# Optimization experiments

Hardware: AMD Instinct MI355X
Metric: run time of the kernel (lower is better)

Reference implementation:

```python
import jax, jax.numpy as jnp
import numpy as np

MEM_LEN = 8


def _conv(x, w, b, stride=1):
    y = jax.lax.conv_general_dilated(x, w, (stride, stride), 'VALID',
                                     dimension_numbers=('NCHW', 'OIHW', 'NCHW'))
    return y + b[None, :, None, None]


def _maxpool3s2(x):
    return jax.lax.reduce_window(x, -jnp.inf, jax.lax.max,
                                 (1, 1, 3, 3), (1, 1, 2, 2), 'VALID')


def _relu(x):
    return jax.nn.relu(x)


def setup_inputs() -> dict:
    key = jax.random.key(0)
    ks = jax.random.split(key, 32)

    def w(i, shape):
        fan_in = float(np.prod(shape[1:]))
        return jax.random.normal(ks[i], shape, jnp.float32) * np.float32(1.0 / np.sqrt(fan_in))

    def bias(i, n):
        return jax.random.normal(ks[i], (n,), jnp.float32) * np.float32(0.01)

    return {
        'x': jax.random.normal(ks[0], (1, 287, 287, 3), jnp.float32),
        'z_reg': jax.random.normal(ks[1], (MEM_LEN, 256, 16), jnp.float32) * 0.1,
        'z_cls': jax.random.normal(ks[2], (MEM_LEN, 256, 16), jnp.float32) * 0.1,
        'bb_w1': w(3, (96, 3, 11, 11)),  'bb_b1': bias(4, 96),
        'bb_w2': w(5, (256, 96, 5, 5)),  'bb_b2': bias(6, 256),
        'bb_w3': w(7, (384, 256, 3, 3)), 'bb_b3': bias(8, 384),
        'bb_w4': w(9, (384, 384, 3, 3)), 'bb_b4': bias(10, 384),
        'bb_w5': w(11, (256, 384, 3, 3)), 'bb_b5': bias(12, 256),
        'wr': w(13, (256, 256, 3, 3)), 'br': bias(14, 256),   # conv_reg2 (conv_search of loc)
        'wc': w(15, (256, 256, 3, 3)), 'bc': bias(16, 256),   # conv_cls2 (conv_search of cls)
        'rh_w1': w(17, (256, 256, 1, 1)), 'rh_b1': bias(18, 256),
        'rh_w2': w(19, (20, 256, 1, 1)),  'rh_b2': bias(20, 20),
        'ch_w1': w(21, (256, 256, 1, 1)), 'ch_b1': bias(22, 256),
        'ch_w2': w(23, (10, 256, 1, 1)),  'ch_b2': bias(24, 10),
        'anc0': jax.random.normal(ks[25], (MEM_LEN, 2205), jnp.float32) * 10.0,
        'anc1': jax.random.normal(ks[26], (MEM_LEN, 2205), jnp.float32) * 10.0,
        'anc2': jax.random.uniform(ks[27], (MEM_LEN, 2205), jnp.float32) * 80.0 + 20.0,
        'anc3': jax.random.uniform(ks[28], (MEM_LEN, 2205), jnp.float32) * 80.0 + 20.0,
    }


def reference(x, z_reg, z_cls,
              bb_w1, bb_b1, bb_w2, bb_b2, bb_w3, bb_b3, bb_w4, bb_b4, bb_w5, bb_b5,
              wr, br, wc, bc,
              rh_w1, rh_b1, rh_w2, rh_b2, ch_w1, ch_b1, ch_w2, ch_b2,
              anc0, anc1, anc2, anc3):
    # Backbone (AlexNet features, BN folded into biases)
    xp = jnp.transpose(x, (0, 3, 1, 2))                     # (1,3,287,287)
    h = _relu(_maxpool3s2(_conv(xp, bb_w1, bb_b1, 2)))      # (1,96,69,69)
    h = _relu(_maxpool3s2(_conv(h, bb_w2, bb_b2)))          # (1,256,32,32)
    h = _relu(_conv(h, bb_w3, bb_b3))                       # (1,384,30,30)
    h = _relu(_conv(h, bb_w4, bb_b4))                       # (1,384,28,28)
    xf = _conv(h, bb_w5, bb_b5)                             # (1,256,26,26)

    c_x = _relu(_conv(xf, wr, br))                          # conv_reg2 -> (1,256,24,24)
    r_x = _relu(_conv(xf, wc, bc))                          # conv_cls2 -> (1,256,24,24)

    def unfold44(t):                                        # (1,256,24,24) -> (256,16,441)
        p = jax.lax.conv_general_dilated_patches(
            t.reshape(256, 1, 24, 24), (4, 4), (1, 1), 'VALID',
            dimension_numbers=('NCHW', 'OIHW', 'NCHW'))     # (256,16,21,21)
        return p.reshape(256, 16, 441)

    c_p = unfold44(c_x)
    r_p = unfold44(r_x)

    # Batched cross-correlation over mem_len templates (fuses the original python loop)
    zr = z_reg.reshape(MEM_LEN, 256, 16)
    zc = z_cls.reshape(MEM_LEN, 256, 16)
    reg_corr = jnp.einsum('ckl,mck->mcl', r_p, zr).reshape(MEM_LEN, 256, 21, 21)
    cls_corr = jnp.einsum('ckl,mck->mcl', c_p, zc).reshape(MEM_LEN, 256, 21, 21)

    cls = _conv(_relu(_conv(cls_corr, ch_w1, ch_b1)), ch_w2, ch_b2)   # (M,10,21,21)
    reg = _conv(_relu(_conv(reg_corr, rh_w1, rh_b1)), rh_w2, rh_b2)   # (M,20,21,21)

    score = jax.nn.softmax(cls.reshape(MEM_LEN, 2, -1), axis=1)       # (M,2,2205)
    delta = reg.reshape(MEM_LEN, 4, -1)                               # (M,4,2205)

    d0 = delta[:, 0, :] * anc2 + anc0
    d1 = delta[:, 1, :] * anc3 + anc1
    d2 = jnp.exp(delta[:, 2, :]) * anc2
    d3 = jnp.exp(delta[:, 3, :]) * anc3
    return (d0, d1, d2, d3, score[:, 1, :])
```

## Files before the change

kernel.cpp:

```cpp
#include <hip/hip_runtime.h>
#include <math.h>

#define TPB 256
static inline int cdiv(int a, int b) { return (a + b - 1) / b; }

typedef short bf8 __attribute__((ext_vector_type(8)));
typedef float f4 __attribute__((ext_vector_type(4)));

__device__ inline float b2f(unsigned short u) {
    union { unsigned int i; float f; } v; v.i = ((unsigned int)u) << 16; return v.f;
}
__device__ inline short f2b(float f) {
    union { float f; unsigned int u; } v; v.f = f;
    unsigned int r = v.u + 0x7FFF + ((v.u >> 16) & 1);
    return (short)(r >> 16);
}

#define OW1   0
#define OW2   67584
#define OW3   722944
#define OW4   1607680
#define OW5   2934784
#define OWRC  3819520
#define OWH1  4999168
#define OZT   5130240
#define OWH2  5195776
#define OBIAS 5203456
#define OACT1 5205504
#define OP1   7062368
#define OACTB 7521472
#define OXF   9520064
#define OCRC  9695168

#define ACT2_OFF  0
#define POOL2_OFF 1083648
#define ACT3_OFF  1347840
#define ACT4_OFF  1695488

__global__ __launch_bounds__(256) void wprep_k(
        const float* __restrict__ bb_w1, const float* __restrict__ bb_w2,
        const float* __restrict__ bb_w3, const float* __restrict__ bb_w4,
        const float* __restrict__ bb_w5,
        const float* __restrict__ wr, const float* __restrict__ wc,
        const float* __restrict__ ch_w1, const float* __restrict__ rh_w1,
        const float* __restrict__ ch_w2, const float* __restrict__ rh_w2,
        const float* __restrict__ z_cls, const float* __restrict__ z_reg,
        const float* __restrict__ br, const float* __restrict__ bc,
        const float* __restrict__ chb1, const float* __restrict__ rhb1,
        const float* __restrict__ x,
        short* __restrict__ W, float* __restrict__ biasf,
        short* __restrict__ xb) {
    __shared__ float lds[3465];
    int bid = blockIdx.x;
    int t = threadIdx.x;

    if (bid < 1792) {
        const float* src;
        short* dst;
        int C, K2, Ot, KwC, orow;
        if (bid < 384)       { int o = bid;        C = 256; K2 = 9;  src = bb_w3 + (size_t)o * 2304; dst = W + OW3;  Ot = 384; KwC = 768;  orow = o; }
        else if (bid < 768)  { int o = bid - 384;  C = 384; K2 = 9;  src = bb_w4 + (size_t)o * 3456; dst = W + OW4;  Ot = 384; KwC = 1152; orow = o; }
        else if (bid < 1024) { int o = bid - 768;  C = 384; K2 = 9;  src = bb_w5 + (size_t)o * 3456; dst = W + OW5;  Ot = 256; KwC = 1152; orow = o; }
        else if (bid < 1280) { int o = bid - 1024; C = 256; K2 = 9;  src = wr    + (size_t)o * 2304; dst = W + OWRC; Ot = 512; KwC = 768;  orow = o; }
        else if (bid < 1536) { int o = bid - 1280; C = 256; K2 = 9;  src = wc    + (size_t)o * 2304; dst = W + OWRC; Ot = 512; KwC = 768;  orow = o + 256; }
        else                 { int o = bid - 1536; C = 96;  K2 = 25; src = bb_w2 + (size_t)o * 2400; dst = W + OW2;  Ot = 256; KwC = 512;  orow = o; }

        int n = C * K2;
        int Cp = C + 1;
        if (K2 == 9) {
            for (int i = t; i < n; i += 256) {
                int kk = i % 9, c = i / 9;
                lds[kk * Cp + c] = src[i];
            }
            __syncthreads();
#pragma unroll
            for (int kk = 0; kk < 9; ++kk) {
                int ki = kk / 3, kj = kk % 3;
                short* rowb = dst + ((size_t)ki * Ot + orow) * KwC + kj * C;
                for (int c = t; c < C; c += 256)
                    rowb[c] = f2b(lds[kk * Cp + c]);
            }
        } else {
            for (int i = t; i < n; i += 256) {
                int kk = i % 25, c = i / 25;
                lds[kk * Cp + c] = src[i];
            }
            __syncthreads();
            for (int kk = 0; kk < 25; ++kk) {
                int ki = kk / 5, kj = kk % 5;
                short* rowb = dst + ((size_t)ki * Ot + orow) * KwC + kj * C;
                if (t < C) rowb[t] = f2b(lds[kk * Cp + t]);
            }
            if (t < 160) {
                int ki = t / 32, kp = 480 + (t & 31);
                dst[((size_t)ki * Ot + orow) * KwC + kp] = 0;
            }
        }
        return;
    }

    int fidx = (bid - 1792) * 256 + t;
    if (fidx < 67584) {
        int k = fidx & 63, o = (fidx >> 6) % 96, ki = fidx / (64 * 96);
        float v = 0.f;
        if (k < 33) v = bb_w1[o * 363 + (k % 3) * 121 + ki * 11 + (k / 3)];
        W[fidx] = f2b(v);
    } else if (fidx < 198656) {
        int i = fidx - 67584;
        const float* src = (i < 65536) ? ch_w1 : rh_w1;
        W[OWH1 + i] = f2b(src[i & 65535]);
    } else if (fidx < 206336) {
        int i = fidx - 198656;
        int o = i >> 8, c = i & 255;
        float v = (o < 10) ? ch_w2[o * 256 + c] : rh_w2[(o - 10) * 256 + c];
        W[OWH2 + i] = f2b(v);
    } else if (fidx < 271872) {
        int i = fidx - 206336;
        const float* src = (i < 32768) ? z_cls : z_reg;
        int j = i & 32767;
        int c = j & 255, k = (j >> 8) & 15, m = j >> 12;
        W[OZT + i] = f2b(src[m * 4096 + c * 16 + k]);
    } else if (fidx < 272896) {
        int i = fidx - 271872;
        const float* src = (i < 256) ? br : (i < 512) ? bc : (i < 768) ? chb1 : rhb1;
        biasf[i] = src[i & 255];
    } else {
        int i = fidx - 272896;
        if (i < 247107) xb[i] = f2b(x[i]);
    }
}

template <int BKC>
__global__ __launch_bounds__(256) void gemm_k(
        const short* __restrict__ in, const short* __restrict__ wt,
        const float* __restrict__ bias, short* __restrict__ out,
        int M, int N, int Wo, int CinW, int Cin,
        int S, int SPR, int aWrap, int bWrap, int KwCp,
        int relu, int msplit, int wsec, int bsec, int nt) {
    constexpr int BK = BKC * 32;
    constexpr int LDW = BK + 8;
    constexpr int CPR = BK / 8;
    constexpr int RPR = 256 / CPR;
    __shared__ short sa[2][64 * LDW];
    __shared__ short sb[2][64 * LDW];

    int bid = blockIdx.x;
    int m0 = (bid / nt) * 64, n0 = (bid % nt) * 64;
    int t = threadIdx.x;
    int lane = t & 63;
    int wid = t >> 6, wm = wid >> 1, wn = wid & 1;
    int sec = (m0 >= msplit) ? 1 : 0;
    const short* wts = wt + (size_t)sec * wsec;
    const float* bs = bias + sec * bsec;

    int rql = t / CPR;
    int ch8 = (t % CPR) * 8;

    const short* pA[BKC];
    const short* pB[BKC];
#pragma unroll
    for (int q = 0; q < BKC; ++q) {
        int mr = m0 + q * RPR + rql; if (mr > M - 1) mr = M - 1;
        int oy = mr / Wo, ox = mr - oy * Wo;
        pA[q] = in + (size_t)oy * CinW + (size_t)ox * Cin + ch8;
        int nr = n0 + q * RPR + rql; if (nr > N - 1) nr = N - 1;
        pB[q] = wts + (size_t)nr * KwCp + ch8;
    }
    int swb = rql * LDW + ch8;

    int arow = (wm * 32 + (lane & 15)) * LDW + (lane >> 4) * 8;
    int brow = (wn * 32 + (lane & 15)) * LDW + (lane >> 4) * 8;

    f4 acc[2][2] = {};
    bf8 va0[BKC], vb0[BKC], va1[BKC], vb1[BKC];
    int srow = 0;

#define LOAD_STEP(vaX, vbX)                                                   \
    do {                                                                      \
        _Pragma("unroll")                                                     \
        for (int q = 0; q < BKC; ++q) {                                       \
            vaX[q] = *(const bf8*)pA[q];                                      \
            vbX[q] = *(const bf8*)pB[q];                                      \
        }                                                                     \
        if (++srow == SPR) {                                                  \
            srow = 0;                                                         \
            _Pragma("unroll")                                                 \
            for (int q = 0; q < BKC; ++q) { pA[q] += aWrap; pB[q] += bWrap; } \
        } else {                                                              \
            _Pragma("unroll")                                                 \
            for (int q = 0; q < BKC; ++q) { pA[q] += BK; pB[q] += BK; }       \
        }                                                                     \
    } while (0)

#define WRITE_LDS(buf, vaX, vbX)                                              \
    do {                                                                      \
        _Pragma("unroll")                                                     \
        for (int q = 0; q < BKC; ++q) {                                       \
            *(bf8*)&sa[buf][swb + q * (RPR * LDW)] = vaX[q];                  \
            *(bf8*)&sb[buf][swb + q * (RPR * LDW)] = vbX[q];                  \
        }                                                                     \
    } while (0)

#define MFMA_STEP(buf)                                                        \
    do {                                                                      \
        const short* A = sa[buf];                                             \
        const short* B = sb[buf];                                             \
        _Pragma("unroll")                                                     \
        for (int kc = 0; kc < BKC; ++kc) {                                    \
            bf8 a0 = *(const bf8*)&A[arow + kc * 32];                         \
            bf8 a1 = *(const bf8*)&A[arow + 16 * LDW + kc * 32];              \
            bf8 b0 = *(const bf8*)&B[brow + kc * 32];                         \
            bf8 b1 = *(const bf8*)&B[brow + 16 * LDW + kc * 32];              \
            acc[0][0] = __builtin_amdgcn_mfma_f32_16x16x32_bf16(a0, b0, acc[0][0], 0, 0, 0); \
            acc[0][1] = __builtin_amdgcn_mfma_f32_16x16x32_bf16(a0, b1, acc[0][1], 0, 0, 0); \
            acc[1][0] = __builtin_amdgcn_mfma_f32_16x16x32_bf16(a1, b0, acc[1][0], 0, 0, 0); \
            acc[1][1] = __builtin_amdgcn_mfma_f32_16x16x32_bf16(a1, b1, acc[1][1], 0, 0, 0); \
        }                                                                     \
    } while (0)

    LOAD_STEP(va0, vb0);
    WRITE_LDS(0, va0, vb0);
    if (S > 1) LOAD_STEP(va1, vb1);
    __syncthreads();

    for (int s = 0; s < S; s += 2) {
        if (s + 2 < S) LOAD_STEP(va0, vb0);
        MFMA_STEP(0);
        if (s + 1 < S) WRITE_LDS(1, va1, vb1);
        __syncthreads();
        if (s + 1 >= S) break;
        if (s + 3 < S) LOAD_STEP(va1, vb1);
        MFMA_STEP(1);
        if (s + 2 < S) WRITE_LDS(0, va0, vb0);
        __syncthreads();
    }
#undef LOAD_STEP
#undef WRITE_LDS
#undef MFMA_STEP

#pragma unroll
    for (int i = 0; i < 2; ++i) {
#pragma unroll
        for (int j = 0; j < 2; ++j) {
            int gm_base = m0 + wm * 32 + i * 16 + (lane >> 4) * 4;
            int gn = n0 + wn * 32 + j * 16 + (lane & 15);
            if (gn < N) {
                float bv = bs[gn];
#pragma unroll
                for (int r = 0; r < 4; ++r) {
                    int gm = gm_base + r;
                    if (gm < M) {
                        float v = acc[i][j][r] + bv;
                        if (relu) v = fmaxf(v, 0.f);
                        out[(size_t)gm * N + gn] = f2b(v);
                    }
                }
            }
        }
    }
}

__global__ void pool_k(const short* __restrict__ in, short* __restrict__ out,
                       int C8, int Win, int Ho) {
    int idx = blockIdx.x * blockDim.x + threadIdx.x;
    int total = Ho * Ho * C8;
    if (idx >= total) return;
    int c8 = idx % C8;
    int p = idx / C8;
    int oy = p / Ho, ox = p % Ho;
    int C = C8 * 8;
    float mx[8];
#pragma unroll
    for (int e = 0; e < 8; ++e) mx[e] = -INFINITY;
#pragma unroll
    for (int ki = 0; ki < 3; ++ki)
#pragma unroll
        for (int kj = 0; kj < 3; ++kj) {
            const bf8 v = *(const bf8*)(in + ((size_t)(oy * 2 + ki) * Win + ox * 2 + kj) * C + c8 * 8);
#pragma unroll
            for (int e = 0; e < 8; ++e) mx[e] = fmaxf(mx[e], b2f((unsigned short)v[e]));
        }
    bf8 o;
#pragma unroll
    for (int e = 0; e < 8; ++e) o[e] = f2b(fmaxf(mx[e], 0.f));
    *(bf8*)(out + (size_t)p * C + c8 * 8) = o;
}

__global__ void dwcorr_k(const short* __restrict__ crcb, const short* __restrict__ zt,
                         short* __restrict__ corr) {
    int idx = blockIdx.x * blockDim.x + threadIdx.x;
    if (idx >= 2 * 903168) return;
    int half = idx / 903168;
    int r = idx - half * 903168;
    int c = r & 255;
    int l = (r >> 8) % 441;
    int mb = r / (441 * 256);
    int y = l / 21, xx = l % 21;
    const short* ip = crcb + half * 256 + (size_t)(y * 24 + xx) * 512 + c;
    const short* zp = zt + half * 32768 + mb * 4096 + c;
    float acc = 0.f;
#pragma unroll
    for (int ki = 0; ki < 4; ++ki)
#pragma unroll
        for (int kj = 0; kj < 4; ++kj)
            acc = fmaf(b2f((unsigned short)ip[(ki * 24 + kj) * 512]),
                       b2f((unsigned short)zp[(ki * 4 + kj) * 256]), acc);
    corr[((size_t)(half * 3584 + mb * 441 + l)) * 256 + c] = f2b(acc);
}

__global__ void head2epi_k(const short* __restrict__ hid, const short* __restrict__ wh2,
                           const float* __restrict__ chb2, const float* __restrict__ rhb2,
                           const float* __restrict__ a0, const float* __restrict__ a1,
                           const float* __restrict__ a2, const float* __restrict__ a3,
                           float* __restrict__ out) {
    const int Ntot = 8 * 2205;
    int idx = blockIdx.x * blockDim.x + threadIdx.x;
    if (idx >= 3 * Ntot) return;
    int g = idx / Ntot;
    int r = idx - g * Ntot;
    int m = r / 2205, j = r % 2205;
    int a = j / 441, pos = j % 441;
    int ml = m * 441 + pos;
    const short* h = hid + (size_t)((g == 0) ? ml : 3584 + ml) * 256;
    int row0, row1;
    float acc0, acc1;
    if (g == 0)      { row0 = a;      row1 = 5 + a;  acc0 = chb2[a];      acc1 = chb2[5 + a];  }
    else if (g == 1) { row0 = 10 + a; row1 = 15 + a; acc0 = rhb2[a];      acc1 = rhb2[5 + a];  }
    else             { row0 = 20 + a; row1 = 25 + a; acc0 = rhb2[10 + a]; acc1 = rhb2[15 + a]; }
    const short* w0 = wh2 + row0 * 256;
    const short* w1 = wh2 + row1 * 256;
    for (int c = 0; c < 256; c += 8) {
        bf8 hv = *(const bf8*)(h + c);
        bf8 w0v = *(const bf8*)(w0 + c);
        bf8 w1v = *(const bf8*)(w1 + c);
#pragma unroll
        for (int e = 0; e < 8; ++e) {
            float hf = b2f((unsigned short)hv[e]);
            acc0 = fmaf(hf, b2f((unsigned short)w0v[e]), acc0);
            acc1 = fmaf(hf, b2f((unsigned short)w1v[e]), acc1);
        }
    }
    if (g == 0) {
        out[4 * Ntot + r] = 1.f / (1.f + expf(acc0 - acc1));
    } else if (g == 1) {
        out[0 * Ntot + r] = fmaf(acc0, a2[r], a0[r]);
        out[1 * Ntot + r] = fmaf(acc1, a3[r], a1[r]);
    } else {
        out[2 * Ntot + r] = expf(acc0) * a2[r];
        out[3 * Ntot + r] = expf(acc1) * a3[r];
    }
}

extern "C" void kernel_launch(void* const* d_in, const int* in_sizes, int n_in,
                              void* d_out, int out_size, void* d_ws, size_t ws_size,
                              hipStream_t stream) {
    const float* x     = (const float*)d_in[0];
    const float* z_reg = (const float*)d_in[1];
    const float* z_cls = (const float*)d_in[2];
    const float* bb_w1 = (const float*)d_in[3];
    const float* bb_b1 = (const float*)d_in[4];
    const float* bb_w2 = (const float*)d_in[5];
    const float* bb_b2 = (const float*)d_in[6];
    const float* bb_w3 = (const float*)d_in[7];
    const float* bb_b3 = (const float*)d_in[8];
    const float* bb_w4 = (const float*)d_in[9];
    const float* bb_b4 = (const float*)d_in[10];
    const float* bb_w5 = (const float*)d_in[11];
    const float* bb_b5 = (const float*)d_in[12];
    const float* wr    = (const float*)d_in[13];
    const float* br    = (const float*)d_in[14];
    const float* wc    = (const float*)d_in[15];
    const float* bc    = (const float*)d_in[16];
    const float* rh_w1 = (const float*)d_in[17];
    const float* rh_b1 = (const float*)d_in[18];
    const float* rh_w2 = (const float*)d_in[19];
    const float* rh_b2 = (const float*)d_in[20];
    const float* ch_w1 = (const float*)d_in[21];
    const float* ch_b1 = (const float*)d_in[22];
    const float* ch_w2 = (const float*)d_in[23];
    const float* ch_b2 = (const float*)d_in[24];
    const float* anc0  = (const float*)d_in[25];
    const float* anc1  = (const float*)d_in[26];
    const float* anc2  = (const float*)d_in[27];
    const float* anc3  = (const float*)d_in[28];

    short* sws  = (short*)d_ws;
    short* W    = sws;
    float* biasf = (float*)(sws + OBIAS);
    short* act1 = sws + OACT1;
    short* pool1 = sws + OP1;
    short* actB = sws + OACTB;
    short* xb   = actB;
    short* act2 = actB + ACT2_OFF;
    short* pool2 = actB + POOL2_OFF;
    short* act3 = actB + ACT3_OFF;
    short* act4 = actB + ACT4_OFF;
    short* corr = actB;
    short* xf   = sws + OXF;
    short* crcb = sws + OCRC;
    short* hid  = act1;

    const int BIG = 1 << 30;

    wprep_k<<<1792 + 2032, 256, 0, stream>>>(
        bb_w1, bb_w2, bb_w3, bb_w4, bb_w5, wr, wc, ch_w1, rh_w1, ch_w2, rh_w2,
        z_cls, z_reg, br, bc, ch_b1, rh_b1, x, W, biasf, xb);

    gemm_k<2><<<302 * 2, 256, 0, stream>>>(
        xb, W + OW1, bb_b1, act1,
        19321, 96, 139, 1722, 6,
        11, 1, 861, 6144, 64, 0, BIG, 0, 0, 2);
    pool_k<<<cdiv(69 * 69 * 12, TPB), TPB, 0, stream>>>(act1, pool1, 12, 139, 69);

    gemm_k<4><<<67 * 4, 256, 0, stream>>>(
        pool1, W + OW2, bb_b2, act2,
        4225, 256, 65, 6624, 96,
        20, 4, 6240, 130688, 512, 0, BIG, 0, 0, 4);
    pool_k<<<cdiv(32 * 32 * 32, TPB), TPB, 0, stream>>>(act2, pool2, 32, 65, 32);

    gemm_k<4><<<15 * 6, 256, 0, stream>>>(
        pool2, W + OW3, bb_b3, act3,
        900, 384, 30, 8192, 256,
        18, 6, 7552, 294272, 768, 1, BIG, 0, 0, 6);

    gemm_k<4><<<13 * 6, 256, 0, stream>>>(
        act3, W + OW4, bb_b4, act4,
        784, 384, 28, 11520, 384,
        27, 9, 10496, 441344, 1152, 1, BIG, 0, 0, 6);

    gemm_k<4><<<11 * 4, 256, 0, stream>>>(
        act4, W + OW5, bb_b5, xf,
        676, 256, 26, 10752, 384,
        27, 9, 9728, 293888, 1152, 0, BIG, 0, 0, 4);

    gemm_k<4><<<9 * 8, 256, 0, stream>>>(
        xf, W + OWRC, biasf, crcb,
        576, 512, 24, 6656, 256,
        18, 6, 6016, 392576, 768, 1, BIG, 0, 0, 8);

    dwcorr_k<<<cdiv(2 * 903168, TPB), TPB, 0, stream>>>(crcb, W + OZT, corr);

    gemm_k<4><<<112 * 4, 256, 0, stream>>>(
        corr, W + OWH1, biasf + 512, hid,
        7112, 256, 7112, 0, 256,
        2, 2, 0, 0, 256, 1, 3584, 65536, 256, 4);

    head2epi_k<<<cdiv(3 * 8 * 2205, TPB), TPB, 0, stream>>>(
        hid, W + OWH2, ch_b2, rh_b2, anc0, anc1, anc2, anc3, (float*)d_out);
}
```

Baseline: 171.4 us.

## Load GEMM tiles directly into LDS with XOR-swizzled layout

Replaces the register-staged global-to-LDS copy in the conv GEMM with direct global_load_lds transfers. The padded LDS rows are dropped in favour of an XOR swizzle of 16-byte chunks, applied on the global read side and undone when fetching MFMA operands. The double-buffer loop is simplified to issue the next stage, compute the current one, then sync. This frees VGPRs and removes the LDS store instructions, but it depends on __syncthreads waiting for the async LDS loads, and each wave's destination must match the lane ordering the direct-to-LDS load implies.

Result: no change. 171.6 us (+0.1%).

```diff
diff --git a/kernel.cpp b/kernel.cpp
--- a/kernel.cpp
+++ b/kernel.cpp
@@ -14,6 +14,12 @@
     union { float f; unsigned int u; } v; v.f = f;
     unsigned int r = v.u + 0x7FFF + ((v.u >> 16) & 1);
     return (short)(r >> 16);
+}
+
+__device__ __forceinline__ void gl_lds16(const short* g, short* l) {
+    __builtin_amdgcn_global_load_lds(
+        reinterpret_cast<const unsigned int*>(g),
+        reinterpret_cast<unsigned int*>(l), 16, 0, 0);
 }
 
 #define OW1   0
@@ -138,11 +144,10 @@
         int S, int SPR, int aWrap, int bWrap, int KwCp,
         int relu, int msplit, int wsec, int bsec, int nt) {
     constexpr int BK = BKC * 32;
-    constexpr int LDW = BK + 8;
     constexpr int CPR = BK / 8;
     constexpr int RPR = 256 / CPR;
-    __shared__ short sa[2][64 * LDW];
-    __shared__ short sb[2][64 * LDW];
+    __shared__ short sa[2][64 * BK];
+    __shared__ short sb[2][64 * BK];
 
     int bid = blockIdx.x;
     int m0 = (bid / nt) * 64, n0 = (bid % nt) * 64;
@@ -154,7 +159,8 @@
     const float* bs = bias + sec * bsec;
 
     int rql = t / CPR;
-    int ch8 = (t % CPR) * 8;
+    int cpos = t % CPR;
+    int gch = (cpos ^ (rql & 7)) * 8;
 
     const short* pA[BKC];
     const short* pB[BKC];
@@ -162,25 +168,25 @@
     for (int q = 0; q < BKC; ++q) {
         int mr = m0 + q * RPR + rql; if (mr > M - 1) mr = M - 1;
         int oy = mr / Wo, ox = mr - oy * Wo;
-        pA[q] = in + (size_t)oy * CinW + (size_t)ox * Cin + ch8;
+        pA[q] = in + (size_t)oy * CinW + (size_t)ox * Cin + gch;
         int nr = n0 + q * RPR + rql; if (nr > N - 1) nr = N - 1;
-        pB[q] = wts + (size_t)nr * KwCp + ch8;
-    }
-    int swb = rql * LDW + ch8;
-
-    int arow = (wm * 32 + (lane & 15)) * LDW + (lane >> 4) * 8;
-    int brow = (wn * 32 + (lane & 15)) * LDW + (lane >> 4) * 8;
+        pB[q] = wts + (size_t)nr * KwCp + gch;
+    }
+    int dstw = wid * 512;
+
+    int cg = lane >> 4, lm7 = lane & 7;
+    int arowb = (wm * 32 + (lane & 15)) * BK;
+    int browb = (wn * 32 + (lane & 15)) * BK;
 
     f4 acc[2][2] = {};
-    bf8 va0[BKC], vb0[BKC], va1[BKC], vb1[BKC];
     int srow = 0;
 
-#define LOAD_STEP(vaX, vbX)                                                   \
+#define ISSUE(buf)                                                            \
     do {                                                                      \
         _Pragma("unroll")                                                     \
         for (int q = 0; q < BKC; ++q) {                                       \
-            vaX[q] = *(const bf8*)pA[q];                                      \
-            vbX[q] = *(const bf8*)pB[q];                                      \
+            gl_lds16(pA[q], &sa[buf][q * (RPR * BK) + dstw]);                 \
+            gl_lds16(pB[q], &sb[buf][q * (RPR * BK) + dstw]);                 \
         }                                                                     \
         if (++srow == SPR) {                                                  \
             srow = 0;                                                         \
@@ -192,25 +198,17 @@
         }                                                                     \
     } while (0)
 
-#define WRITE_LDS(buf, vaX, vbX)                                              \
-    do {                                                                      \
-        _Pragma("unroll")                                                     \
-        for (int q = 0; q < BKC; ++q) {                                       \
-            *(bf8*)&sa[buf][swb + q * (RPR * LDW)] = vaX[q];                  \
-            *(bf8*)&sb[buf][swb + q * (RPR * LDW)] = vbX[q];                  \
-        }                                                                     \
-    } while (0)
-
 #define MFMA_STEP(buf)                                                        \
     do {                                                                      \
         const short* A = sa[buf];                                             \
         const short* B = sb[buf];                                             \
         _Pragma("unroll")                                                     \
         for (int kc = 0; kc < BKC; ++kc) {                                    \
-            bf8 a0 = *(const bf8*)&A[arow + kc * 32];                         \
-            bf8 a1 = *(const bf8*)&A[arow + 16 * LDW + kc * 32];              \
-            bf8 b0 = *(const bf8*)&B[brow + kc * 32];                         \
-            bf8 b1 = *(const bf8*)&B[brow + 16 * LDW + kc * 32];              \
+            int ch = (((kc << 2) | cg) ^ lm7) * 8;                            \
+            bf8 a0 = *(const bf8*)&A[arowb + ch];                             \
+            bf8 a1 = *(const bf8*)&A[arowb + 16 * BK + ch];                   \
+            bf8 b0 = *(const bf8*)&B[browb + ch];                             \
+            bf8 b1 = *(const bf8*)&B[browb + 16 * BK + ch];                   \
             acc[0][0] = __builtin_amdgcn_mfma_f32_16x16x32_bf16(a0, b0, acc[0][0], 0, 0, 0); \
             acc[0][1] = __builtin_amdgcn_mfma_f32_16x16x32_bf16(a0, b1, acc[0][1], 0, 0, 0); \
             acc[1][0] = __builtin_amdgcn_mfma_f32_16x16x32_bf16(a1, b0, acc[1][0], 0, 0, 0); \
@@ -218,24 +216,15 @@
         }                                                                     \
     } while (0)
 
-    LOAD_STEP(va0, vb0);
-    WRITE_LDS(0, va0, vb0);
-    if (S > 1) LOAD_STEP(va1, vb1);
+    ISSUE(0);
     __syncthreads();
 
-    for (int s = 0; s < S; s += 2) {
-        if (s + 2 < S) LOAD_STEP(va0, vb0);
-        MFMA_STEP(0);
-        if (s + 1 < S) WRITE_LDS(1, va1, vb1);
+    for (int s = 0; s < S; ++s) {
+        if (s + 1 < S) ISSUE((s + 1) & 1);
+        MFMA_STEP(s & 1);
         __syncthreads();
-        if (s + 1 >= S) break;
-        if (s + 3 < S) LOAD_STEP(va1, vb1);
-        MFMA_STEP(1);
-        if (s + 2 < S) WRITE_LDS(0, va0, vb0);
-        __syncthreads();
-    }
-#undef LOAD_STEP
-#undef WRITE_LDS
+    }
+#undef ISSUE
 #undef MFMA_STEP
 
 #pragma unroll
```

## Split K dimension across two workgroup halves for small conv GEMMs

Applied to the files above, without the earlier changes.

Adds an intra-block split-K option to the implicit-GEMM kernel: with KSPLIT=2 the block has 512 threads, each 256-thread half accumulates half of the K steps into its own LDS buffers, and the partial sums are reduced through shared memory before the epilogue. The four small conv layers (conv3-5 and the search conv), which launch fewer blocks than the GPU has compute units, now use it so more waves run per tile. The pipeline is also restructured from two register staging sets to a single one-step prefetch. In exchange, LDS use per block doubles, there is extra reduction traffic and a barrier, and the simpler prefetch may hide less latency.

Measured after the change: 155.1 us. 1.11x faster.

```diff
diff --git a/kernel.cpp b/kernel.cpp
--- a/kernel.cpp
+++ b/kernel.cpp
@@ -130,8 +130,8 @@
     }
 }
 
-template <int BKC>
-__global__ __launch_bounds__(256) void gemm_k(
+template <int BKC, int KSPLIT>
+__global__ __launch_bounds__(KSPLIT * 256) void gemm_k(
         const short* __restrict__ in, const short* __restrict__ wt,
         const float* __restrict__ bias, short* __restrict__ out,
         int M, int N, int Wo, int CinW, int Cin,
@@ -141,20 +141,33 @@
     constexpr int LDW = BK + 8;
     constexpr int CPR = BK / 8;
     constexpr int RPR = 256 / CPR;
-    __shared__ short sa[2][64 * LDW];
-    __shared__ short sb[2][64 * LDW];
+    __shared__ short sa[KSPLIT][2][64 * LDW];
+    __shared__ short sb[KSPLIT][2][64 * LDW];
 
     int bid = blockIdx.x;
     int m0 = (bid / nt) * 64, n0 = (bid % nt) * 64;
     int t = threadIdx.x;
-    int lane = t & 63;
-    int wid = t >> 6, wm = wid >> 1, wn = wid & 1;
+    int wg = (KSPLIT == 2) ? (t >> 8) : 0;
+    int t8 = t & 255;
+    int lane = t8 & 63;
+    int wid = t8 >> 6, wm = wid >> 1, wn = wid & 1;
     int sec = (m0 >= msplit) ? 1 : 0;
     const short* wts = wt + (size_t)sec * wsec;
     const float* bs = bias + sec * bsec;
 
-    int rql = t / CPR;
-    int ch8 = (t % CPR) * 8;
+    int Sh, n1, nReal;
+    if (KSPLIT == 2) {
+        Sh = (S + 1) >> 1;
+        n1 = wg * Sh;
+        nReal = wg ? (S - Sh) : Sh;
+    } else { Sh = S; n1 = 0; nReal = S; }
+    int wraps = n1 / SPR;
+    int srow = n1 % SPR;
+    int offA0 = wraps * aWrap + (n1 - wraps) * BK;
+    int offB0 = wraps * bWrap + (n1 - wraps) * BK;
+
+    int rql = t8 / CPR;
+    int ch8 = (t8 % CPR) * 8;
 
     const short* pA[BKC];
     const short* pB[BKC];
@@ -162,9 +175,9 @@
     for (int q = 0; q < BKC; ++q) {
         int mr = m0 + q * RPR + rql; if (mr > M - 1) mr = M - 1;
         int oy = mr / Wo, ox = mr - oy * Wo;
-        pA[q] = in + (size_t)oy * CinW + (size_t)ox * Cin + ch8;
+        pA[q] = in + (size_t)oy * CinW + (size_t)ox * Cin + ch8 + offA0;
         int nr = n0 + q * RPR + rql; if (nr > N - 1) nr = N - 1;
-        pB[q] = wts + (size_t)nr * KwCp + ch8;
+        pB[q] = wts + (size_t)nr * KwCp + ch8 + offB0;
     }
     int swb = rql * LDW + ch8;
 
@@ -172,15 +185,14 @@
     int brow = (wn * 32 + (lane & 15)) * LDW + (lane >> 4) * 8;
 
     f4 acc[2][2] = {};
-    bf8 va0[BKC], vb0[BKC], va1[BKC], vb1[BKC];
-    int srow = 0;
-
-#define LOAD_STEP(vaX, vbX)                                                   \
+    bf8 va[BKC], vb[BKC];
+
+#define LOAD_STEP()                                                           \
     do {                                                                      \
         _Pragma("unroll")                                                     \
         for (int q = 0; q < BKC; ++q) {                                       \
-            vaX[q] = *(const bf8*)pA[q];                                      \
-            vbX[q] = *(const bf8*)pB[q];                                      \
+            va[q] = *(const bf8*)pA[q];                                       \
+            vb[q] = *(const bf8*)pB[q];                                       \
         }                                                                     \
         if (++srow == SPR) {                                                  \
             srow = 0;                                                         \
@@ -192,19 +204,19 @@
         }                                                                     \
     } while (0)
 
-#define WRITE_LDS(buf, vaX, vbX)                                              \
+#define WRITE_LDS(buf)                                                        \
     do {                                                                      \
         _Pragma("unroll")                                                     \
         for (int q = 0; q < BKC; ++q) {                                       \
-            *(bf8*)&sa[buf][swb + q * (RPR * LDW)] = vaX[q];                  \
-            *(bf8*)&sb[buf][swb + q * (RPR * LDW)] = vbX[q];                  \
+            *(bf8*)&sa[wg][buf][swb + q * (RPR * LDW)] = va[q];               \
+            *(bf8*)&sb[wg][buf][swb + q * (RPR * LDW)] = vb[q];               \
         }                                                                     \
     } while (0)
 
 #define MFMA_STEP(buf)                                                        \
     do {                                                                      \
-        const short* A = sa[buf];                                             \
-        const short* B = sb[buf];                                             \
+        const short* A = sa[wg][buf];                                         \
+        const short* B = sb[wg][buf];                                         \
         _Pragma("unroll")                                                     \
         for (int kc = 0; kc < BKC; ++kc) {                                    \
             bf8 a0 = *(const bf8*)&A[arow + kc * 32];                         \
@@ -218,25 +230,46 @@
         }                                                                     \
     } while (0)
 
-    LOAD_STEP(va0, vb0);
-    WRITE_LDS(0, va0, vb0);
-    if (S > 1) LOAD_STEP(va1, vb1);
+    if (nReal > 0) {
+        LOAD_STEP();
+        WRITE_LDS(0);
+    }
     __syncthreads();
 
-    for (int s = 0; s < S; s += 2) {
-        if (s + 2 < S) LOAD_STEP(va0, vb0);
-        MFMA_STEP(0);
-        if (s + 1 < S) WRITE_LDS(1, va1, vb1);
-        __syncthreads();
-        if (s + 1 >= S) break;
-        if (s + 3 < S) LOAD_STEP(va1, vb1);
-        MFMA_STEP(1);
-        if (s + 2 < S) WRITE_LDS(0, va0, vb0);
+    for (int sloc = 0; sloc < Sh; ++sloc) {
+        int cur = sloc & 1;
+        bool act = sloc < nReal;
+        bool pre = (sloc + 1 < nReal);
+        if (pre) LOAD_STEP();
+        if (act) MFMA_STEP(cur);
+        if (pre) WRITE_LDS(cur ^ 1);
         __syncthreads();
     }
 #undef LOAD_STEP
 #undef WRITE_LDS
 #undef MFMA_STEP
+
+    if (KSPLIT == 2) {
+        float* red = (float*)&sa[0][0][0];
+        if (wg == 1) {
+#pragma unroll
+            for (int i = 0; i < 2; ++i)
+#pragma unroll
+                for (int j = 0; j < 2; ++j)
+#pragma unroll
+                    for (int r = 0; r < 4; ++r)
+                        red[t8 * 16 + (i * 2 + j) * 4 + r] = acc[i][j][r];
+        }
+        __syncthreads();
+        if (wg == 1) return;
+#pragma unroll
+        for (int i = 0; i < 2; ++i)
+#pragma unroll
+            for (int j = 0; j < 2; ++j)
+#pragma unroll
+                for (int r = 0; r < 4; ++r)
+                    acc[i][j][r] += red[t8 * 16 + (i * 2 + j) * 4 + r];
+    }
 
 #pragma unroll
     for (int i = 0; i < 2; ++i) {
@@ -406,41 +439,41 @@
         bb_w1, bb_w2, bb_w3, bb_w4, bb_w5, wr, wc, ch_w1, rh_w1, ch_w2, rh_w2,
         z_cls, z_reg, br, bc, ch_b1, rh_b1, x, W, biasf, xb);
 
-    gemm_k<2><<<302 * 2, 256, 0, stream>>>(
+    gemm_k<2, 1><<<302 * 2, 256, 0, stream>>>(
         xb, W + OW1, bb_b1, act1,
         19321, 96, 139, 1722, 6,
         11, 1, 861, 6144, 64, 0, BIG, 0, 0, 2);
     pool_k<<<cdiv(69 * 69 * 12, TPB), TPB, 0, stream>>>(act1, pool1, 12, 139, 69);
 
-    gemm_k<4><<<67 * 4, 256, 0, stream>>>(
+    gemm_k<4, 1><<<67 * 4, 256, 0, stream>>>(
         pool1, W + OW2, bb_b2, act2,
         4225, 256, 65, 6624, 96,
         20, 4, 6240, 130688, 512, 0, BIG, 0, 0, 4);
     pool_k<<<cdiv(32 * 32 * 32, TPB), TPB, 0, stream>>>(act2, pool2, 32, 65, 32);
 
-    gemm_k<4><<<15 * 6, 256, 0, stream>>>(
+    gemm_k<4, 2><<<15 * 6, 512, 0, stream>>>(
         pool2, W + OW3, bb_b3, act3,
         900, 384, 30, 8192, 256,
         18, 6, 7552, 294272, 768, 1, BIG, 0, 0, 6);
 
-    gemm_k<4><<<13 * 6, 256, 0, stream>>>(
+    gemm_k<4, 2><<<13 * 6, 512, 0, stream>>>(
         act3, W + OW4, bb_b4, act4,
         784, 384, 28, 11520, 384,
         27, 9, 10496, 441344, 1152, 1, BIG, 0, 0, 6);
 
-    gemm_k<4><<<11 * 4, 256, 0, stream>>>(
+    gemm_k<4, 2><<<11 * 4, 512, 0, stream>>>(
         act4, W + OW5, bb_b5, xf,
         676, 256, 26, 10752, 384,
         27, 9, 9728, 293888, 1152, 0, BIG, 0, 0, 4);
 
-    gemm_k<4><<<9 * 8, 256, 0, stream>>>(
+    gemm_k<4, 2><<<9 * 8, 512, 0, stream>>>(
         xf, W + OWRC, biasf, crcb,
         576, 512, 24, 6656, 256,
         18, 6, 6016, 392576, 768, 1, BIG, 0, 0, 8);
 
     dwcorr_k<<<cdiv(2 * 903168, TPB), TPB, 0, stream>>>(crcb, W + OZT, corr);
 
-    gemm_k<4><<<112 * 4, 256, 0, stream>>>(
+    gemm_k<4, 1><<<112 * 4, 256, 0, stream>>>(
         corr, W + OWH1, biasf + 512, hid,
         7112, 256, 7112, 0, 256,
         2, 2, 0, 0, 256, 1, 3584, 65536, 256, 4);
```
